# Optimization experiments

Hardware: AMD Instinct MI355X
Metric: run time of the kernel (lower is better)

Reference implementation:

```python
import jax, jax.numpy as jnp
import numpy as np

N = 100000      # nodes
E = 1600000     # edges (avg degree 16)
F_IN = 128      # in_feats
H = 128         # n_hidden
C = 40          # n_classes


def setup_inputs() -> dict:
    key = jax.random.key(0)
    ks = jax.random.split(key, 11)
    s = 0.05
    return {
        "x": jax.random.normal(ks[0], (N, F_IN), jnp.float32),
        "edge_index": jax.random.randint(ks[1], (2, E), 0, N, jnp.int32),
        # layer 1: SAGEConv(F_IN, H); lin_l has bias, lin_r has none (PyG default)
        "Wl1": jax.random.normal(ks[2], (F_IN, H), jnp.float32) * s,
        "bl1": jnp.zeros((H,), jnp.float32),
        "Wr1": jax.random.normal(ks[3], (F_IN, H), jnp.float32) * s,
        # layer 2: SAGEConv(H, H)
        "Wl2": jax.random.normal(ks[4], (H, H), jnp.float32) * s,
        "bl2": jnp.zeros((H,), jnp.float32),
        "Wr2": jax.random.normal(ks[5], (H, H), jnp.float32) * s,
        # layer 3: SAGEConv(H, C)
        "Wl3": jax.random.normal(ks[6], (H, C), jnp.float32) * s,
        "bl3": jnp.zeros((C,), jnp.float32),
        "Wr3": jax.random.normal(ks[7], (H, C), jnp.float32) * s,
    }


def _sage_conv(x, src, dst, Wl, bl, Wr):
    # PyG SAGEConv (aggr='mean', root_weight=True):
    #   out[i] = lin_l( mean_{j->i} x[j] ) + lin_r( x[i] )
    msgs = x[src]                                            # [E, d] irregular gather
    agg = jax.ops.segment_sum(msgs, dst, num_segments=N)     # [N, d]
    deg = jax.ops.segment_sum(jnp.ones((src.shape[0], 1), x.dtype), dst,
                              num_segments=N)                # [N, 1]
    agg = agg / jnp.maximum(deg, 1.0)                        # mean aggregation
    return agg @ Wl + bl + x @ Wr


def reference(x, edge_index, Wl1, bl1, Wr1, Wl2, bl2, Wr2, Wl3, bl3, Wr3):
    src, dst = edge_index[0], edge_index[1]
    h = jax.nn.relu(_sage_conv(x, src, dst, Wl1, bl1, Wr1))   # dropout is identity in eval
    h = jax.nn.relu(_sage_conv(h, src, dst, Wl2, bl2, Wr2))
    return _sage_conv(h, src, dst, Wl3, bl3, Wr3)             # [N, C]
```

## Files before the change

### kernel.cpp

```cpp
#include <hip/hip_runtime.h>

using u16 = unsigned short;
using u32 = unsigned int;
typedef __attribute__((ext_vector_type(8))) short short8;
typedef __attribute__((ext_vector_type(4))) float f32x4;

static inline int idiv_up(long a, long b) { return (int)((a + b - 1) / b); }

#define NBUCK 256
#define ECHUNK 8192
#define CAPE 9216

__device__ __forceinline__ float bflo(u32 p) { return __uint_as_float(p << 16); }
__device__ __forceinline__ float bfhi(u32 p) { return __uint_as_float(p & 0xffff0000u); }
__device__ __forceinline__ u32 f2bf1(float f) {
    u32 x = __float_as_uint(f);
    return (x + 0x7fffu + ((x >> 16) & 1u)) >> 16;
}
__device__ __forceinline__ u32 pack2(float lo, float hi) {
    return f2bf1(lo) | (f2bf1(hi) << 16);
}

__global__ __launch_bounds__(256) void k_cast(const float* __restrict__ x,
                                              u32* __restrict__ xb, long nelem) {
    long i = ((long)blockIdx.x * 256 + threadIdx.x) * 8;
    if (i >= nelem) return;
    float4 v0 = *(const float4*)(x + i);
    float4 v1 = *(const float4*)(x + i + 4);
    uint4 o;
    o.x = pack2(v0.x, v0.y);
    o.y = pack2(v0.z, v0.w);
    o.z = pack2(v1.x, v1.y);
    o.w = pack2(v1.z, v1.w);
    *(uint4*)(xb + (i >> 1)) = o;
}

__global__ __launch_bounds__(256) void k_wprep(const float* __restrict__ Wl,
                                               const float* __restrict__ Wr,
                                               u16* __restrict__ wp) {
    const int gid = blockIdx.x * 256 + threadIdx.x;
    if (gid >= 64 * 64) return;
    const int tile = gid >> 6, l = gid & 63;
    const int t = tile >> 3, s = tile & 7;
    const int n = t * 16 + (l & 15);
    const int k0 = s * 32 + (l >> 4) * 8;
    u32 w[4];
#pragma unroll
    for (int p = 0; p < 4; ++p) {
        const int ka = k0 + 2 * p, kb = ka + 1;
        const float va = (ka < 128) ? Wl[ka * 128 + n] : Wr[(ka - 128) * 128 + n];
        const float vb = (kb < 128) ? Wl[kb * 128 + n] : Wr[(kb - 128) * 128 + n];
        w[p] = pack2(va, vb);
    }
    uint4 o = {w[0], w[1], w[2], w[3]};
    *(uint4*)(wp + (size_t)gid * 8) = o;
}

__global__ __launch_bounds__(256) void k_wprep3(const float* __restrict__ Wl,
                                                const float* __restrict__ Wr,
                                                u16* __restrict__ wp) {
    const int gid = blockIdx.x * 256 + threadIdx.x;
    if (gid >= 20 * 64) return;
    const int tile = gid >> 6, l = gid & 63;
    const int t = tile >> 2, s = tile & 3;
    const int c = t * 16 + (l & 15);
    const int k0 = s * 32 + (l >> 4) * 8;
    u32 w[4];
#pragma unroll
    for (int p = 0; p < 4; ++p) {
        const int ka = k0 + 2 * p, kb = ka + 1;
        const float va = (c < 40) ? Wl[ka * 40 + c] : Wr[ka * 40 + (c - 40)];
        const float vb = (c < 40) ? Wl[kb * 40 + c] : Wr[kb * 40 + (c - 40)];
        w[p] = pack2(va, vb);
    }
    uint4 o = {w[0], w[1], w[2], w[3]};
    *(uint4*)(wp + (size_t)gid * 8) = o;
}


__global__ __launch_bounds__(256) void k_pcount(const int* __restrict__ dst,
                                                int* __restrict__ pcA,
                                                int E, int rangeSize, int nPB) {
    __shared__ int s_cnt[NBUCK];
    s_cnt[threadIdx.x] = 0;
    __syncthreads();
    const long e0 = (long)blockIdx.x * ECHUNK;
#pragma unroll 4
    for (int j = 0; j < ECHUNK / 256; ++j) {
        const long e = e0 + j * 256 + threadIdx.x;
        if (e < E) {
            const int d = __builtin_nontemporal_load(&dst[e]);
            atomicAdd(&s_cnt[d / rangeSize], 1);
        }
    }
    __syncthreads();
    pcA[threadIdx.x * nPB + blockIdx.x] = s_cnt[threadIdx.x];
}

__global__ __launch_bounds__(256) void k_pwrite(const int* __restrict__ src,
                                                const int* __restrict__ dst,
                                                const int* __restrict__ pcB,
                                                u32* __restrict__ stage,
                                                int E, int rangeSize, int nPB) {
    __shared__ int s_base[NBUCK];
    __shared__ int s_off[NBUCK];
    s_base[threadIdx.x] = pcB[threadIdx.x * nPB + blockIdx.x];
    s_off[threadIdx.x] = 0;
    __syncthreads();
    const long e0 = (long)blockIdx.x * ECHUNK;
#pragma unroll 4
    for (int j = 0; j < ECHUNK / 256; ++j) {
        const long e = e0 + j * 256 + threadIdx.x;
        if (e < E) {
            const int d = __builtin_nontemporal_load(&dst[e]);
            const int s = __builtin_nontemporal_load(&src[e]);
            const int b = d / rangeSize;
            const int r = d - b * rangeSize;
            const int p = atomicAdd(&s_off[b], 1);
            stage[s_base[b] + p] = (u32)s | ((u32)r << 17);
        }
    }
}

__global__ __launch_bounds__(256) void k_csrlds(const u32* __restrict__ stage,
                                                const int* __restrict__ pcB,
                                                int* __restrict__ rowptr,
                                                float* __restrict__ invd,
                                                int* __restrict__ col,
                                                int rangeSize, int nPB, int n) {
    __shared__ int s_cnt[512];
    __shared__ int s_cur[512];
    __shared__ int s_col[CAPE];
    __shared__ int wt[4];
    const int b = blockIdx.x;
    const int t = threadIdx.x;
    const int g0 = b * rangeSize;
    const int base = pcB[b * nPB];
    const int end = pcB[(b + 1) * nPB];

    for (int i = t; i < rangeSize; i += 256) s_cnt[i] = 0;
    __syncthreads();

    for (int i = base + t; i < end; i += 256)
        atomicAdd(&s_cnt[stage[i] >> 17], 1);
    __syncthreads();

    const int i0 = 2 * t, i1 = 2 * t + 1;
    const int c0 = (i0 < rangeSize) ? s_cnt[i0] : 0;
    const int c1 = (i1 < rangeSize) ? s_cnt[i1] : 0;
    const int sum = c0 + c1;
    const int lane = t & 63, wid = t >> 6;
    int incl = sum;
    for (int off = 1; off < 64; off <<= 1) {
        int u = __shfl_up(incl, off, 64);
        if (lane >= off) incl += u;
    }
    if (lane == 63) wt[wid] = incl;
    __syncthreads();
    int woff = 0;
    for (int w = 0; w < wid; ++w) woff += wt[w];
    const int excl = woff + incl - sum;
    if (i0 < rangeSize) {
        s_cur[i0] = excl;
        const int g = g0 + i0;
        if (g <= n) rowptr[g] = base + excl;
        if (g < n) invd[g] = 1.0f / fmaxf((float)c0, 1.0f);
    }
    if (i1 < rangeSize) {
        s_cur[i1] = excl + c0;
        const int g = g0 + i1;
        if (g <= n) rowptr[g] = base + excl + c0;
        if (g < n) invd[g] = 1.0f / fmaxf((float)c1, 1.0f);
    }
    __syncthreads();

    for (int i = base + t; i < end; i += 256) {
        const u32 v = stage[i];
        const int p = atomicAdd(&s_cur[v >> 17], 1);
        s_col[p] = (int)(v & 0x1FFFFu);
    }
    __syncthreads();

    const int cnt = end - base;
    for (int i = t; i < cnt; i += 256) col[base + i] = s_col[i];
}

__global__ __launch_bounds__(256) void k_scan1(const int* __restrict__ degi,
                                               int* __restrict__ rowptr,
                                               float* __restrict__ invd,
                                               int* __restrict__ partials, int n) {
    __shared__ int wt[4];
    const int base = blockIdx.x * 1024 + threadIdx.x * 4;
    int v[4];
    int sum = 0;
#pragma unroll
    for (int j = 0; j < 4; ++j) {
        int g = base + j;
        v[j] = (g < n) ? degi[g] : 0;
        sum += v[j];
    }
    const int lane = threadIdx.x & 63;
    const int wid = threadIdx.x >> 6;
    int incl = sum;
    for (int off = 1; off < 64; off <<= 1) {
        int t = __shfl_up(incl, off, 64);
        if (lane >= off) incl += t;
    }
    if (lane == 63) wt[wid] = incl;
    __syncthreads();
    int woff = 0;
    for (int w = 0; w < wid; ++w) woff += wt[w];
    int run = woff + incl - sum;
#pragma unroll
    for (int j = 0; j < 4; ++j) {
        int g = base + j;
        if (g < n) {
            rowptr[g] = run;
            invd[g] = 1.0f / fmaxf((float)v[j], 1.0f);
        }
        run += v[j];
    }
    if (threadIdx.x == 255) partials[blockIdx.x] = woff + incl;
}

__global__ __launch_bounds__(256) void k_scan2(int* p, int nb) {
    __shared__ int wt[4];
    __shared__ int carry;
    if (threadIdx.x == 0) carry = 0;
    __syncthreads();
    for (int bs = 0; bs < nb; bs += 256) {
        const int i = bs + threadIdx.x;
        int v = (i < nb) ? p[i] : 0;
        const int lane = threadIdx.x & 63;
        const int wid = threadIdx.x >> 6;
        int incl = v;
        for (int off = 1; off < 64; off <<= 1) {
            int t = __shfl_up(incl, off, 64);
            if (lane >= off) incl += t;
        }
        if (lane == 63) wt[wid] = incl;
        __syncthreads();
        int woff = 0;
        for (int w = 0; w < wid; ++w) woff += wt[w];
        int excl = carry + woff + incl - v;
        if (i < nb) p[i] = excl;
        __syncthreads();
        if (threadIdx.x == 255) carry += woff + incl;
        __syncthreads();
    }
}

__global__ __launch_bounds__(256) void k_scan3(int* __restrict__ rowptr,
                                               const int* __restrict__ partials,
                                               int n, int E) {
    const int base = blockIdx.x * 1024;
    const int add = partials[blockIdx.x];
    for (int i = threadIdx.x; i < 1024; i += 256) {
        int g = base + i;
        if (g < n) rowptr[g] += add;
    }
    if (blockIdx.x == 0 && threadIdx.x == 0) rowptr[n] = E;
}

#define ACC4(A, V)                                                     \
    A.x += bflo(V.x); A.y += bfhi(V.x); A.z += bflo(V.y); A.w += bfhi(V.y);

__global__ __launch_bounds__(256) void k_aggb(const u16* __restrict__ xb,
                                              const int* __restrict__ rowptr,
                                              const int* __restrict__ col,
                                              const float* __restrict__ invd,
                                              u16* __restrict__ aggb, int n) {
    const int t = blockIdx.x * 256 + threadIdx.x;
    const int node = t >> 5;
    if (node >= n) return;
    const int l = t & 31;
    const int s0 = rowptr[node], s1 = rowptr[node + 1];
    float4 a0 = {0.f, 0.f, 0.f, 0.f};
    float4 a1 = {0.f, 0.f, 0.f, 0.f};
    for (int cb = s0; cb < s1; cb += 32) {
        const int cnt = min(32, s1 - cb);
        const int cc = (cb + l < s1) ? col[cb + l] : 0;
        int j = 0;
        for (; j + 8 <= cnt; j += 8) {
            const int n0 = __shfl(cc, j, 32);
            const int n1 = __shfl(cc, j + 1, 32);
            const int n2 = __shfl(cc, j + 2, 32);
            const int n3 = __shfl(cc, j + 3, 32);
            const int n4 = __shfl(cc, j + 4, 32);
            const int n5 = __shfl(cc, j + 5, 32);
            const int n6 = __shfl(cc, j + 6, 32);
            const int n7 = __shfl(cc, j + 7, 32);
            const uint2 v0 = *(const uint2*)(xb + (size_t)n0 * 128 + 4 * l);
            const uint2 v1 = *(const uint2*)(xb + (size_t)n1 * 128 + 4 * l);
            const uint2 v2 = *(const uint2*)(xb + (size_t)n2 * 128 + 4 * l);
            const uint2 v3 = *(const uint2*)(xb + (size_t)n3 * 128 + 4 * l);
            const uint2 v4 = *(const uint2*)(xb + (size_t)n4 * 128 + 4 * l);
            const uint2 v5 = *(const uint2*)(xb + (size_t)n5 * 128 + 4 * l);
            const uint2 v6 = *(const uint2*)(xb + (size_t)n6 * 128 + 4 * l);
            const uint2 v7 = *(const uint2*)(xb + (size_t)n7 * 128 + 4 * l);
            ACC4(a0, v0); ACC4(a1, v1); ACC4(a0, v2); ACC4(a1, v3);
            ACC4(a0, v4); ACC4(a1, v5); ACC4(a0, v6); ACC4(a1, v7);
        }
        for (; j + 4 <= cnt; j += 4) {
            const int n0 = __shfl(cc, j, 32);
            const int n1 = __shfl(cc, j + 1, 32);
            const int n2 = __shfl(cc, j + 2, 32);
            const int n3 = __shfl(cc, j + 3, 32);
            const uint2 v0 = *(const uint2*)(xb + (size_t)n0 * 128 + 4 * l);
            const uint2 v1 = *(const uint2*)(xb + (size_t)n1 * 128 + 4 * l);
            const uint2 v2 = *(const uint2*)(xb + (size_t)n2 * 128 + 4 * l);
            const uint2 v3 = *(const uint2*)(xb + (size_t)n3 * 128 + 4 * l);
            ACC4(a0, v0); ACC4(a1, v1); ACC4(a0, v2); ACC4(a1, v3);
        }
        for (; j < cnt; ++j) {
            const int nn = __shfl(cc, j, 32);
            const uint2 v = *(const uint2*)(xb + (size_t)nn * 128 + 4 * l);
            ACC4(a0, v);
        }
    }
    const float inv = invd[node];
    uint2 o;
    o.x = pack2((a0.x + a1.x) * inv, (a0.y + a1.y) * inv);
    o.y = pack2((a0.z + a1.z) * inv, (a0.w + a1.w) * inv);
    *(uint2*)(aggb + (size_t)node * 128 + 4 * l) = o;
}

__global__ __launch_bounds__(256, 4) void k_mmf(const u16* __restrict__ aggb,
                                                const u16* __restrict__ xrb,
                                                const u16* __restrict__ wp,
                                                const float* __restrict__ bl,
                                                u16* __restrict__ outb, int n) {
    __shared__ __align__(16) u16 s_a[64][264];
    const int row0 = blockIdx.x * 64;
    const int tid = threadIdx.x;

#pragma unroll
    for (int it = 0; it < 8; ++it) {
        const int idx = tid + it * 256;
        const int r = idx >> 5, c8 = idx & 31;
        const int row = row0 + r;
        uint4 v = {0u, 0u, 0u, 0u};
        if (row < n) {
            v = (c8 < 16) ? *(const uint4*)(aggb + (size_t)row * 128 + c8 * 8)
                          : *(const uint4*)(xrb + (size_t)row * 128 + (c8 - 16) * 8);
        }
        *(uint4*)(&s_a[r][c8 * 8]) = v;
    }
    __syncthreads();

    const int l = tid & 63;
    const int w = tid >> 6;
    const int rloc = w * 16 + (l & 15);
    const int q = l >> 4;

    short8 afr[8];
#pragma unroll
    for (int s = 0; s < 8; ++s)
        afr[s] = *(const short8*)(&s_a[rloc][s * 32 + q * 8]);

    f32x4 acc[8];
#pragma unroll
    for (int t = 0; t < 8; ++t) acc[t] = (f32x4){0.f, 0.f, 0.f, 0.f};

#pragma unroll
    for (int t = 0; t < 8; ++t) {
#pragma unroll
        for (int s = 0; s < 8; ++s) {
            const short8 b = *(const short8*)(wp + ((size_t)(t * 8 + s) * 64 + l) * 8);
            acc[t] = __builtin_amdgcn_mfma_f32_16x16x32_bf16(afr[s], b, acc[t], 0, 0, 0);
        }
    }

    const int rowb = row0 + w * 16 + q * 4;
#pragma unroll
    for (int t = 0; t < 8; ++t) {
        const float bias = bl[t * 16 + (l & 15)];
#pragma unroll
        for (int r = 0; r < 4; ++r) {
            const int row = rowb + r;
            if (row < n) {
                const float o = fmaxf(acc[t][r] + bias, 0.f);
                outb[(size_t)row * 128 + t * 16 + (l & 15)] = (u16)f2bf1(o);
            }
        }
    }
}

__global__ __launch_bounds__(256, 4) void k_mm40f(const u16* __restrict__ hb,
                                                  const u16* __restrict__ wp,
                                                  const float* __restrict__ bl,
                                                  u16* __restrict__ t40b,
                                                  float* __restrict__ r40, int n) {
    __shared__ __align__(16) u16 s_a[64][136];
    const int row0 = blockIdx.x * 64;
    const int tid = threadIdx.x;

#pragma unroll
    for (int it = 0; it < 4; ++it) {
        const int idx = tid + it * 256;
        const int r = idx >> 4, c8 = idx & 15;
        const int row = row0 + r;
        uint4 v = {0u, 0u, 0u, 0u};
        if (row < n) v = *(const uint4*)(hb + (size_t)row * 128 + c8 * 8);
        *(uint4*)(&s_a[r][c8 * 8]) = v;
    }
    __syncthreads();

    const int l = tid & 63;
    const int w = tid >> 6;
    const int rloc = w * 16 + (l & 15);
    const int q = l >> 4;

    short8 afr[4];
#pragma unroll
    for (int s = 0; s < 4; ++s)
        afr[s] = *(const short8*)(&s_a[rloc][s * 32 + q * 8]);

    f32x4 acc[5];
#pragma unroll
    for (int t = 0; t < 5; ++t) acc[t] = (f32x4){0.f, 0.f, 0.f, 0.f};

#pragma unroll
    for (int t = 0; t < 5; ++t) {
#pragma unroll
        for (int s = 0; s < 4; ++s) {
            const short8 b = *(const short8*)(wp + ((size_t)(t * 4 + s) * 64 + l) * 8);
            acc[t] = __builtin_amdgcn_mfma_f32_16x16x32_bf16(afr[s], b, acc[t], 0, 0, 0);
        }
    }

    const int rowb = row0 + w * 16 + q * 4;
#pragma unroll
    for (int t = 0; t < 5; ++t) {
        const int c = t * 16 + (l & 15);
        const float bias = (c >= 40) ? bl[c - 40] : 0.f;
#pragma unroll
        for (int r = 0; r < 4; ++r) {
            const int row = rowb + r;
            if (row < n) {
                if (c < 40)
                    t40b[(size_t)row * 40 + c] = (u16)f2bf1(acc[t][r]);
                else
                    r40[(size_t)row * 40 + (c - 40)] = acc[t][r] + bias;
            }
        }
    }
}

__global__ __launch_bounds__(256) void k_agg40(const u16* __restrict__ t40b,
                                               const float* __restrict__ r40,
                                               const int* __restrict__ rowptr,
                                               const int* __restrict__ col,
                                               const float* __restrict__ invd,
                                               float* __restrict__ out, int n) {
    const int tt = blockIdx.x * 256 + threadIdx.x;
    const int node = tt >> 4;
    if (node >= n) return;
    const int l = tt & 15;
    const bool act = l < 10;
    const int s0 = rowptr[node], s1 = rowptr[node + 1];
    float4 a0 = {0.f, 0.f, 0.f, 0.f};
    float4 a1 = {0.f, 0.f, 0.f, 0.f};
    for (int cb = s0; cb < s1; cb += 16) {
        const int cnt = min(16, s1 - cb);
        const int cc = (cb + l < s1) ? col[cb + l] : 0;
        int j = 0;
        for (; j + 4 <= cnt; j += 4) {
            const int n0 = __shfl(cc, j, 16);
            const int n1 = __shfl(cc, j + 1, 16);
            const int n2 = __shfl(cc, j + 2, 16);
            const int n3 = __shfl(cc, j + 3, 16);
            if (act) {
                const uint2 v0 = *(const uint2*)(t40b + (size_t)n0 * 40 + 4 * l);
                const uint2 v1 = *(const uint2*)(t40b + (size_t)n1 * 40 + 4 * l);
                const uint2 v2 = *(const uint2*)(t40b + (size_t)n2 * 40 + 4 * l);
                const uint2 v3 = *(const uint2*)(t40b + (size_t)n3 * 40 + 4 * l);
                ACC4(a0, v0); ACC4(a1, v1); ACC4(a0, v2); ACC4(a1, v3);
            }
        }
        for (; j < cnt; ++j) {
            const int nn = __shfl(cc, j, 16);
            if (act) {
                const uint2 v = *(const uint2*)(t40b + (size_t)nn * 40 + 4 * l);
                ACC4(a0, v);
            }
        }
    }
    if (act) {
        const float inv = invd[node];
        const float4 rv = *(const float4*)(r40 + (size_t)node * 40 + 4 * l);
        float4 o;
        o.x = fmaf(a0.x + a1.x, inv, rv.x);
        o.y = fmaf(a0.y + a1.y, inv, rv.y);
        o.z = fmaf(a0.z + a1.z, inv, rv.z);
        o.w = fmaf(a0.w + a1.w, inv, rv.w);
        *(float4*)(out + (size_t)node * 40 + 4 * l) = o;
    }
}

extern "C" void kernel_launch(void* const* d_in, const int* in_sizes, int n_in,
                              void* d_out, int out_size, void* d_ws, size_t ws_size,
                              hipStream_t stream) {
    const float* x   = (const float*)d_in[0];
    const int*   ei  = (const int*)d_in[1];
    const float* Wl1 = (const float*)d_in[2];
    const float* bl1 = (const float*)d_in[3];
    const float* Wr1 = (const float*)d_in[4];
    const float* Wl2 = (const float*)d_in[5];
    const float* bl2 = (const float*)d_in[6];
    const float* Wr2 = (const float*)d_in[7];
    const float* Wl3 = (const float*)d_in[8];
    const float* bl3 = (const float*)d_in[9];
    const float* Wr3 = (const float*)d_in[10];
    float* out = (float*)d_out;

    const int N = in_sizes[0] / 128;
    const int E = in_sizes[1] / 2;
    const int* src = ei;
    const int* dst = ei + E;

    auto align1k = [](size_t v) { return (v + 1023) & ~(size_t)1023; };
    const size_t NB16 = (size_t)N * 128 * sizeof(u16);

    const int nPB = idiv_up(E, ECHUNK);
    const int M = NBUCK * nPB;

    char* ws = (char*)d_ws;
    size_t off = 0;
    int*   scratch  = (int*)(ws + off);   off += align1k((size_t)N * 4);
    float* invd     = (float*)(ws + off); off += align1k((size_t)N * 4);
    int*   rowptr   = (int*)(ws + off);   off += align1k((size_t)(N + 1) * 4);
    int*   partials = (int*)(ws + off);   off += align1k(4096);
    int*   pcA      = (int*)(ws + off);   off += align1k((size_t)M * 4);
    int*   pcB      = (int*)(ws + off);   off += align1k((size_t)(M + 1) * 4);
    u16*   wp1      = (u16*)(ws + off);   off += align1k(64 * 1024);
    u16*   wp2      = (u16*)(ws + off);   off += align1k(64 * 1024);
    u16*   wp3      = (u16*)(ws + off);   off += align1k(20 * 1024);
    int*   col      = (int*)(ws + off);   off += align1k((size_t)E * 4);
    u32*   stage    = (u32*)(ws + off);   off += align1k((size_t)E * 4);
    u16*   aggb     = (u16*)(ws + off);   off += align1k(NB16);
    u16*   xb       = (u16*)(ws + off);   off += align1k(NB16);
    char*  regionY  = (ws + off);         off += align1k(NB16);
    u16*   h1b  = (u16*)regionY;
    u16*   h2b  = xb;
    u16*   t40b = (u16*)regionY;
    float* r40  = (float*)(regionY + align1k((size_t)N * 40 * sizeof(u16)));

    const int scanBlocksE = idiv_up(M, 1024);
    const int castBlocks  = idiv_up((long)N * 128, 2048);
    const int aggBlocks   = idiv_up((long)N * 32, 256);
    const int agg40Blk    = idiv_up((long)N * 16, 256);
    const int mmBlocks    = idiv_up(N, 64);
    const int rangeSize   = idiv_up(N, NBUCK);

    k_cast<<<castBlocks, 256, 0, stream>>>(x, (u32*)xb, (long)N * 128);
    k_wprep<<<16, 256, 0, stream>>>(Wl1, Wr1, wp1);
    k_wprep<<<16, 256, 0, stream>>>(Wl2, Wr2, wp2);
    k_wprep3<<<5, 256, 0, stream>>>(Wl3, Wr3, wp3);

    k_pcount<<<nPB, 256, 0, stream>>>(dst, pcA, E, rangeSize, nPB);
    k_scan1<<<scanBlocksE, 256, 0, stream>>>(pcA, pcB, (float*)scratch, partials, M);
    k_scan2<<<1, 256, 0, stream>>>(partials, scanBlocksE);
    k_scan3<<<scanBlocksE, 256, 0, stream>>>(pcB, partials, M, E);
    k_pwrite<<<nPB, 256, 0, stream>>>(src, dst, pcB, stage, E, rangeSize, nPB);
    k_csrlds<<<NBUCK, 256, 0, stream>>>(stage, pcB, rowptr, invd, col, rangeSize, nPB, N);

    k_aggb<<<aggBlocks, 256, 0, stream>>>(xb, rowptr, col, invd, aggb, N);
    k_mmf<<<mmBlocks, 256, 0, stream>>>(aggb, xb, wp1, bl1, h1b, N);

    k_aggb<<<aggBlocks, 256, 0, stream>>>(h1b, rowptr, col, invd, aggb, N);
    k_mmf<<<mmBlocks, 256, 0, stream>>>(aggb, h1b, wp2, bl2, h2b, N);

    k_mm40f<<<mmBlocks, 256, 0, stream>>>(h2b, wp3, bl3, t40b, r40, N);
    k_agg40<<<agg40Blk, 256, 0, stream>>>(t40b, r40, rowptr, col, invd, out, N);
}
```

Baseline: 311.2 us.

## Single-pass bucket CSR build with atomic cursors; 16-lane uint4 aggregation

```diff
diff --git a/kernel.cpp b/kernel.cpp
--- a/kernel.cpp
+++ b/kernel.cpp
@@ -2,6 +2,7 @@
 
 using u16 = unsigned short;
 using u32 = unsigned int;
+using u8 = unsigned char;
 typedef __attribute__((ext_vector_type(8))) short short8;
 typedef __attribute__((ext_vector_type(4))) float f32x4;
 
@@ -77,57 +78,68 @@
     *(uint4*)(wp + (size_t)gid * 8) = o;
 }
 
-
-__global__ __launch_bounds__(256) void k_pcount(const int* __restrict__ dst,
-                                                int* __restrict__ pcA,
-                                                int E, int rangeSize, int nPB) {
+__global__ __launch_bounds__(256) void k_bucket(const int* __restrict__ src,
+                                                const int* __restrict__ dst,
+                                                int* __restrict__ cursor,
+                                                u32* __restrict__ stage,
+                                                int E, int rangeSize) {
+    __shared__ u32 s_pay[ECHUNK];
+    __shared__ u8 s_bk[ECHUNK];
     __shared__ int s_cnt[NBUCK];
-    s_cnt[threadIdx.x] = 0;
-    __syncthreads();
-    const long e0 = (long)blockIdx.x * ECHUNK;
-#pragma unroll 4
-    for (int j = 0; j < ECHUNK / 256; ++j) {
-        const long e = e0 + j * 256 + threadIdx.x;
-        if (e < E) {
-            const int d = __builtin_nontemporal_load(&dst[e]);
-            atomicAdd(&s_cnt[d / rangeSize], 1);
-        }
-    }
-    __syncthreads();
-    pcA[threadIdx.x * nPB + blockIdx.x] = s_cnt[threadIdx.x];
-}
-
-__global__ __launch_bounds__(256) void k_pwrite(const int* __restrict__ src,
-                                                const int* __restrict__ dst,
-                                                const int* __restrict__ pcB,
-                                                u32* __restrict__ stage,
-                                                int E, int rangeSize, int nPB) {
     __shared__ int s_base[NBUCK];
     __shared__ int s_off[NBUCK];
-    s_base[threadIdx.x] = pcB[threadIdx.x * nPB + blockIdx.x];
-    s_off[threadIdx.x] = 0;
+    s_cnt[threadIdx.x] = 0;
     __syncthreads();
     const long e0 = (long)blockIdx.x * ECHUNK;
-#pragma unroll 4
-    for (int j = 0; j < ECHUNK / 256; ++j) {
-        const long e = e0 + j * 256 + threadIdx.x;
-        if (e < E) {
-            const int d = __builtin_nontemporal_load(&dst[e]);
-            const int s = __builtin_nontemporal_load(&src[e]);
-            const int b = d / rangeSize;
-            const int r = d - b * rangeSize;
-            const int p = atomicAdd(&s_off[b], 1);
-            stage[s_base[b] + p] = (u32)s | ((u32)r << 17);
-        }
-    }
+    const int cnt = (int)(((long)E - e0 < ECHUNK) ? (long)E - e0 : ECHUNK);
+    for (int j = threadIdx.x; j < cnt; j += 256) {
+        const int d = __builtin_nontemporal_load(&dst[e0 + j]);
+        const int s = __builtin_nontemporal_load(&src[e0 + j]);
+        const int b = d / rangeSize;
+        s_pay[j] = (u32)s | ((u32)(d - b * rangeSize) << 17);
+        s_bk[j] = (u8)b;
+        atomicAdd(&s_cnt[b], 1);
+    }
+    __syncthreads();
+    {
+        const int c = s_cnt[threadIdx.x];
+        s_base[threadIdx.x] = c ? atomicAdd(&cursor[threadIdx.x], c) : 0;
+        s_off[threadIdx.x] = 0;
+    }
+    __syncthreads();
+    for (int j = threadIdx.x; j < cnt; j += 256) {
+        const int b = s_bk[j];
+        const int p = atomicAdd(&s_off[b], 1);
+        stage[(size_t)b * CAPE + s_base[b] + p] = s_pay[j];
+    }
+}
+
+__global__ __launch_bounds__(256) void k_bscan(const int* __restrict__ cursor,
+                                               int* __restrict__ bbase, int E) {
+    __shared__ int wt[4];
+    const int t = threadIdx.x;
+    const int v = cursor[t];
+    const int lane = t & 63, wid = t >> 6;
+    int incl = v;
+    for (int off = 1; off < 64; off <<= 1) {
+        int u = __shfl_up(incl, off, 64);
+        if (lane >= off) incl += u;
+    }
+    if (lane == 63) wt[wid] = incl;
+    __syncthreads();
+    int woff = 0;
+    for (int w = 0; w < wid; ++w) woff += wt[w];
+    bbase[t] = woff + incl - v;
+    if (t == 255) bbase[256] = woff + incl;
 }
 
 __global__ __launch_bounds__(256) void k_csrlds(const u32* __restrict__ stage,
-                                                const int* __restrict__ pcB,
+                                                const int* __restrict__ bcnt,
+                                                const int* __restrict__ bbase,
                                                 int* __restrict__ rowptr,
                                                 float* __restrict__ invd,
                                                 int* __restrict__ col,
-                                                int rangeSize, int nPB, int n) {
+                                                int rangeSize, int n) {
     __shared__ int s_cnt[512];
     __shared__ int s_cur[512];
     __shared__ int s_col[CAPE];
@@ -135,14 +147,15 @@
     const int b = blockIdx.x;
     const int t = threadIdx.x;
     const int g0 = b * rangeSize;
-    const int base = pcB[b * nPB];
-    const int end = pcB[(b + 1) * nPB];
+    const size_t rd = (size_t)b * CAPE;
+    const int cntb = bcnt[b];
+    const int gbase = bbase[b];
 
     for (int i = t; i < rangeSize; i += 256) s_cnt[i] = 0;
     __syncthreads();
 
-    for (int i = base + t; i < end; i += 256)
-        atomicAdd(&s_cnt[stage[i] >> 17], 1);
+    for (int i = t; i < cntb; i += 256)
+        atomicAdd(&s_cnt[stage[rd + i] >> 17], 1);
     __syncthreads();
 
     const int i0 = 2 * t, i1 = 2 * t + 1;
@@ -163,107 +176,30 @@
     if (i0 < rangeSize) {
         s_cur[i0] = excl;
         const int g = g0 + i0;
-        if (g <= n) rowptr[g] = base + excl;
+        if (g <= n) rowptr[g] = gbase + excl;
         if (g < n) invd[g] = 1.0f / fmaxf((float)c0, 1.0f);
     }
     if (i1 < rangeSize) {
         s_cur[i1] = excl + c0;
         const int g = g0 + i1;
-        if (g <= n) rowptr[g] = base + excl + c0;
+        if (g <= n) rowptr[g] = gbase + excl + c0;
         if (g < n) invd[g] = 1.0f / fmaxf((float)c1, 1.0f);
     }
     __syncthreads();
 
-    for (int i = base + t; i < end; i += 256) {
-        const u32 v = stage[i];
+    for (int i = t; i < cntb; i += 256) {
+        const u32 v = stage[rd + i];
         const int p = atomicAdd(&s_cur[v >> 17], 1);
         s_col[p] = (int)(v & 0x1FFFFu);
     }
     __syncthreads();
 
-    const int cnt = end - base;
-    for (int i = t; i < cnt; i += 256) col[base + i] = s_col[i];
-}
-
-__global__ __launch_bounds__(256) void k_scan1(const int* __restrict__ degi,
-                                               int* __restrict__ rowptr,
-                                               float* __restrict__ invd,
-                                               int* __restrict__ partials, int n) {
-    __shared__ int wt[4];
-    const int base = blockIdx.x * 1024 + threadIdx.x * 4;
-    int v[4];
-    int sum = 0;
-#pragma unroll
-    for (int j = 0; j < 4; ++j) {
-        int g = base + j;
-        v[j] = (g < n) ? degi[g] : 0;
-        sum += v[j];
-    }
-    const int lane = threadIdx.x & 63;
-    const int wid = threadIdx.x >> 6;
-    int incl = sum;
-    for (int off = 1; off < 64; off <<= 1) {
-        int t = __shfl_up(incl, off, 64);
-        if (lane >= off) incl += t;
-    }
-    if (lane == 63) wt[wid] = incl;
-    __syncthreads();
-    int woff = 0;
-    for (int w = 0; w < wid; ++w) woff += wt[w];
-    int run = woff + incl - sum;
-#pragma unroll
-    for (int j = 0; j < 4; ++j) {
-        int g = base + j;
-        if (g < n) {
-            rowptr[g] = run;
-            invd[g] = 1.0f / fmaxf((float)v[j], 1.0f);
-        }
-        run += v[j];
-    }
-    if (threadIdx.x == 255) partials[blockIdx.x] = woff + incl;
-}
-
-__global__ __launch_bounds__(256) void k_scan2(int* p, int nb) {
-    __shared__ int wt[4];
-    __shared__ int carry;
-    if (threadIdx.x == 0) carry = 0;
-    __syncthreads();
-    for (int bs = 0; bs < nb; bs += 256) {
-        const int i = bs + threadIdx.x;
-        int v = (i < nb) ? p[i] : 0;
-        const int lane = threadIdx.x & 63;
-        const int wid = threadIdx.x >> 6;
-        int incl = v;
-        for (int off = 1; off < 64; off <<= 1) {
-            int t = __shfl_up(incl, off, 64);
-            if (lane >= off) incl += t;
-        }
-        if (lane == 63) wt[wid] = incl;
-        __syncthreads();
-        int woff = 0;
-        for (int w = 0; w < wid; ++w) woff += wt[w];
-        int excl = carry + woff + incl - v;
-        if (i < nb) p[i] = excl;
-        __syncthreads();
-        if (threadIdx.x == 255) carry += woff + incl;
-        __syncthreads();
-    }
-}
-
-__global__ __launch_bounds__(256) void k_scan3(int* __restrict__ rowptr,
-                                               const int* __restrict__ partials,
-                                               int n, int E) {
-    const int base = blockIdx.x * 1024;
-    const int add = partials[blockIdx.x];
-    for (int i = threadIdx.x; i < 1024; i += 256) {
-        int g = base + i;
-        if (g < n) rowptr[g] += add;
-    }
-    if (blockIdx.x == 0 && threadIdx.x == 0) rowptr[n] = E;
-}
-
-#define ACC4(A, V)                                                     \
-    A.x += bflo(V.x); A.y += bfhi(V.x); A.z += bflo(V.y); A.w += bfhi(V.y);
+    for (int i = t; i < cntb; i += 256) col[gbase + i] = s_col[i];
+}
+
+#define ACC8(A, B, V)                                                          \
+    A.x += bflo(V.x); A.y += bfhi(V.x); A.z += bflo(V.y); A.w += bfhi(V.y);    \
+    B.x += bflo(V.z); B.y += bfhi(V.z); B.z += bflo(V.w); B.w += bfhi(V.w);
 
 __global__ __launch_bounds__(256) void k_aggb(const u16* __restrict__ xb,
                                               const int* __restrict__ rowptr,
@@ -271,58 +207,41 @@
                                               const float* __restrict__ invd,
                                               u16* __restrict__ aggb, int n) {
     const int t = blockIdx.x * 256 + threadIdx.x;
-    const int node = t >> 5;
+    const int node = t >> 4;
     if (node >= n) return;
-    const int l = t & 31;
+    const int l = t & 15;
     const int s0 = rowptr[node], s1 = rowptr[node + 1];
-    float4 a0 = {0.f, 0.f, 0.f, 0.f};
-    float4 a1 = {0.f, 0.f, 0.f, 0.f};
-    for (int cb = s0; cb < s1; cb += 32) {
-        const int cnt = min(32, s1 - cb);
+    float4 eA0 = {0.f, 0.f, 0.f, 0.f}, eA1 = {0.f, 0.f, 0.f, 0.f};
+    float4 eB0 = {0.f, 0.f, 0.f, 0.f}, eB1 = {0.f, 0.f, 0.f, 0.f};
+    for (int cb = s0; cb < s1; cb += 16) {
+        const int cnt = min(16, s1 - cb);
         const int cc = (cb + l < s1) ? col[cb + l] : 0;
         int j = 0;
-        for (; j + 8 <= cnt; j += 8) {
-            const int n0 = __shfl(cc, j, 32);
-            const int n1 = __shfl(cc, j + 1, 32);
-            const int n2 = __shfl(cc, j + 2, 32);
-            const int n3 = __shfl(cc, j + 3, 32);
-            const int n4 = __shfl(cc, j + 4, 32);
-            const int n5 = __shfl(cc, j + 5, 32);
-            const int n6 = __shfl(cc, j + 6, 32);
-            const int n7 = __shfl(cc, j + 7, 32);
-            const uint2 v0 = *(const uint2*)(xb + (size_t)n0 * 128 + 4 * l);
-            const uint2 v1 = *(const uint2*)(xb + (size_t)n1 * 128 + 4 * l);
-            const uint2 v2 = *(const uint2*)(xb + (size_t)n2 * 128 + 4 * l);
-            const uint2 v3 = *(const uint2*)(xb + (size_t)n3 * 128 + 4 * l);
-            const uint2 v4 = *(const uint2*)(xb + (size_t)n4 * 128 + 4 * l);
-            const uint2 v5 = *(const uint2*)(xb + (size_t)n5 * 128 + 4 * l);
-            const uint2 v6 = *(const uint2*)(xb + (size_t)n6 * 128 + 4 * l);
-            const uint2 v7 = *(const uint2*)(xb + (size_t)n7 * 128 + 4 * l);
-            ACC4(a0, v0); ACC4(a1, v1); ACC4(a0, v2); ACC4(a1, v3);
-            ACC4(a0, v4); ACC4(a1, v5); ACC4(a0, v6); ACC4(a1, v7);
-        }
         for (; j + 4 <= cnt; j += 4) {
-            const int n0 = __shfl(cc, j, 32);
-            const int n1 = __shfl(cc, j + 1, 32);
-            const int n2 = __shfl(cc, j + 2, 32);
-            const int n3 = __shfl(cc, j + 3, 32);
-            const uint2 v0 = *(const uint2*)(xb + (size_t)n0 * 128 + 4 * l);
-            const uint2 v1 = *(const uint2*)(xb + (size_t)n1 * 128 + 4 * l);
-            const uint2 v2 = *(const uint2*)(xb + (size_t)n2 * 128 + 4 * l);
-            const uint2 v3 = *(const uint2*)(xb + (size_t)n3 * 128 + 4 * l);
-            ACC4(a0, v0); ACC4(a1, v1); ACC4(a0, v2); ACC4(a1, v3);
+            const int n0 = __shfl(cc, j, 16);
+            const int n1 = __shfl(cc, j + 1, 16);
+            const int n2 = __shfl(cc, j + 2, 16);
+            const int n3 = __shfl(cc, j + 3, 16);
+            const uint4 v0 = *(const uint4*)(xb + (size_t)n0 * 128 + 8 * l);
+            const uint4 v1 = *(const uint4*)(xb + (size_t)n1 * 128 + 8 * l);
+            const uint4 v2 = *(const uint4*)(xb + (size_t)n2 * 128 + 8 * l);
+            const uint4 v3 = *(const uint4*)(xb + (size_t)n3 * 128 + 8 * l);
+            ACC8(eA0, eA1, v0); ACC8(eB0, eB1, v1);
+            ACC8(eA0, eA1, v2); ACC8(eB0, eB1, v3);
         }
         for (; j < cnt; ++j) {
-            const int nn = __shfl(cc, j, 32);
-            const uint2 v = *(const uint2*)(xb + (size_t)nn * 128 + 4 * l);
-            ACC4(a0, v);
+            const int nn = __shfl(cc, j, 16);
+            const uint4 v = *(const uint4*)(xb + (size_t)nn * 128 + 8 * l);
+            ACC8(eA0, eA1, v);
         }
     }
     const float inv = invd[node];
-    uint2 o;
-    o.x = pack2((a0.x + a1.x) * inv, (a0.y + a1.y) * inv);
-    o.y = pack2((a0.z + a1.z) * inv, (a0.w + a1.w) * inv);
-    *(uint2*)(aggb + (size_t)node * 128 + 4 * l) = o;
+    uint4 o;
+    o.x = pack2((eA0.x + eB0.x) * inv, (eA0.y + eB0.y) * inv);
+    o.y = pack2((eA0.z + eB0.z) * inv, (eA0.w + eB0.w) * inv);
+    o.z = pack2((eA1.x + eB1.x) * inv, (eA1.y + eB1.y) * inv);
+    o.w = pack2((eA1.z + eB1.z) * inv, (eA1.w + eB1.w) * inv);
+    *(uint4*)(aggb + (size_t)node * 128 + 8 * l) = o;
 }
 
 __global__ __launch_bounds__(256, 4) void k_mmf(const u16* __restrict__ aggb,
@@ -446,6 +365,9 @@
         }
     }
 }
+
+#define ACC4(A, V)                                                     \
+    A.x += bflo(V.x); A.y += bfhi(V.x); A.z += bflo(V.y); A.w += bfhi(V.y);
 
 __global__ __launch_bounds__(256) void k_agg40(const u16* __restrict__ t40b,
                                                const float* __restrict__ r40,
@@ -522,22 +444,17 @@
     auto align1k = [](size_t v) { return (v + 1023) & ~(size_t)1023; };
     const size_t NB16 = (size_t)N * 128 * sizeof(u16);
 
-    const int nPB = idiv_up(E, ECHUNK);
-    const int M = NBUCK * nPB;
-
     char* ws = (char*)d_ws;
     size_t off = 0;
-    int*   scratch  = (int*)(ws + off);   off += align1k((size_t)N * 4);
     float* invd     = (float*)(ws + off); off += align1k((size_t)N * 4);
     int*   rowptr   = (int*)(ws + off);   off += align1k((size_t)(N + 1) * 4);
-    int*   partials = (int*)(ws + off);   off += align1k(4096);
-    int*   pcA      = (int*)(ws + off);   off += align1k((size_t)M * 4);
-    int*   pcB      = (int*)(ws + off);   off += align1k((size_t)(M + 1) * 4);
+    int*   cursor   = (int*)(ws + off);   off += align1k(NBUCK * 4);
+    int*   bbase    = (int*)(ws + off);   off += align1k((NBUCK + 1) * 4);
     u16*   wp1      = (u16*)(ws + off);   off += align1k(64 * 1024);
     u16*   wp2      = (u16*)(ws + off);   off += align1k(64 * 1024);
     u16*   wp3      = (u16*)(ws + off);   off += align1k(20 * 1024);
     int*   col      = (int*)(ws + off);   off += align1k((size_t)E * 4);
-    u32*   stage    = (u32*)(ws + off);   off += align1k((size_t)E * 4);
+    u32*   stage    = (u32*)(ws + off);   off += align1k((size_t)NBUCK * CAPE * 4);
     u16*   aggb     = (u16*)(ws + off);   off += align1k(NB16);
     u16*   xb       = (u16*)(ws + off);   off += align1k(NB16);
     char*  regionY  = (ws + off);         off += align1k(NB16);
@@ -546,24 +463,23 @@
     u16*   t40b = (u16*)regionY;
     float* r40  = (float*)(regionY + align1k((size_t)N * 40 * sizeof(u16)));
 
-    const int scanBlocksE = idiv_up(M, 1024);
-    const int castBlocks  = idiv_up((long)N * 128, 2048);
-    const int aggBlocks   = idiv_up((long)N * 32, 256);
-    const int agg40Blk    = idiv_up((long)N * 16, 256);
-    const int mmBlocks    = idiv_up(N, 64);
-    const int rangeSize   = idiv_up(N, NBUCK);
+    const int nPB        = idiv_up(E, ECHUNK);
+    const int castBlocks = idiv_up((long)N * 128, 2048);
+    const int aggBlocks  = idiv_up((long)N * 16, 256);
+    const int agg40Blk   = idiv_up((long)N * 16, 256);
+    const int mmBlocks   = idiv_up(N, 64);
+    const int rangeSize  = idiv_up(N, NBUCK);
 
     k_cast<<<castBlocks, 256, 0, stream>>>(x, (u32*)xb, (long)N * 128);
     k_wprep<<<16, 256, 0, stream>>>(Wl1, Wr1, wp1);
     k_wprep<<<16, 256, 0, stream>>>(Wl2, Wr2, wp2);
     k_wprep3<<<5, 256, 0, stream>>>(Wl3, Wr3, wp3);
 
-    k_pcount<<<nPB, 256, 0, stream>>>(dst, pcA, E, rangeSize, nPB);
-    k_scan1<<<scanBlocksE, 256, 0, stream>>>(pcA, pcB, (float*)scratch, partials, M);
-    k_scan2<<<1, 256, 0, stream>>>(partials, scanBlocksE);
-    k_scan3<<<scanBlocksE, 256, 0, stream>>>(pcB, partials, M, E);
-    k_pwrite<<<nPB, 256, 0, stream>>>(src, dst, pcB, stage, E, rangeSize, nPB);
-    k_csrlds<<<NBUCK, 256, 0, stream>>>(stage, pcB, rowptr, invd, col, rangeSize, nPB, N);
+    hipMemsetAsync(cursor, 0, NBUCK * sizeof(int), stream);
+    k_bucket<<<nPB, 256, 0, stream>>>(src, dst, cursor, stage, E, rangeSize);
+    k_bscan<<<1, 256, 0, stream>>>(cursor, bbase, E);
+    k_csrlds<<<NBUCK, 256, 0, stream>>>(stage, cursor, bbase, rowptr, invd, col,
+                                        rangeSize, N);
 
     k_aggb<<<aggBlocks, 256, 0, stream>>>(xb, rowptr, col, invd, aggb, N);
     k_mmf<<<mmBlocks, 256, 0, stream>>>(aggb, xb, wp1, bl1, h1b, N);
```

Result: faster. 301.4 us (-3.1%).
